# Optimization experiments

Hardware: AMD Instinct MI355X
Metric: run time of the kernel (lower is better)

The kernel has to match this reference:

```python
import jax, jax.numpy as jnp
import numpy as np

N = 8192      # nodes
IN = 1433     # input_feat_dim
H1 = 256      # hidden_dim1
H2 = 128      # hidden_dim2
EPS = 1e-5    # BatchNorm1d eps
NEG = -9e15   # GAT mask value
SLOPE = 0.2   # leaky_relu negative slope (gamma)


def setup_inputs() -> dict:
    key = jax.random.key(0)
    ks = jax.random.split(key, 8)
    x = jax.random.normal(ks[0], (N, H2), dtype=jnp.float32)
    u = jax.random.uniform(ks[1], (N, N), dtype=jnp.float32)
    adj = jnp.where(u > 0.999, jnp.float32(0.01), jnp.float32(0.0))
    def w(k, shape):
        fan = shape[0]
        return jax.random.normal(k, shape, dtype=jnp.float32) / jnp.sqrt(jnp.float32(fan))
    return {
        "x": x,
        "adj": adj,
        "W_att": w(ks[2], (H2, H2)),
        "a_att": w(ks[3], (2 * H2, 1)),
        "W_fd1": w(ks[4], (H2, H1)),
        "bn1_g": jnp.ones((H1,), jnp.float32),
        "bn1_b": jnp.zeros((H1,), jnp.float32),
        "W_fd2": w(ks[5], (H1, IN)),
        "bn2_g": jnp.ones((IN,), jnp.float32),
        "bn2_b": jnp.zeros((IN,), jnp.float32),
        "W_sd1": w(ks[6], (H2, H1)),
        "bn3_g": jnp.ones((H1,), jnp.float32),
        "bn3_b": jnp.zeros((H1,), jnp.float32),
    }


def batchnorm(h, g, b):
    # BatchNorm1d training-mode forward: batch stats, biased variance
    m = h.mean(axis=0)
    v = ((h - m) ** 2).mean(axis=0)
    return (h - m) * jax.lax.rsqrt(v + EPS) * g + b


def reference(x, adj, W_att, a_att, W_fd1, bn1_g, bn1_b, W_fd2, bn2_g, bn2_b,
              W_sd1, bn3_g, bn3_b):
    # --- GraphAttentionLayer (concat=False, dropout=0) ---
    Wh = x @ W_att                       # [N, H2]
    f1 = Wh @ a_att[:H2]                 # [N, 1]
    f2 = Wh @ a_att[H2:]                 # [N, 1]
    e = jax.nn.leaky_relu(f1 + f2.T, SLOPE)          # [N, N]
    att = jnp.where(adj > 0, e, jnp.float32(NEG))
    att = jax.nn.softmax(att, axis=1)
    z = att @ Wh                         # condensed encoder output [N, H2]
    # --- feature decoder branch ---
    h1 = jax.nn.relu(adj @ (z @ W_fd1))  # GCN: adj @ (X W), relu
    h1 = batchnorm(h1, bn1_g, bn1_b)
    feat = jax.nn.relu(adj @ (h1 @ W_fd2))
    feat = batchnorm(feat, bn2_g, bn2_b)
    # --- structure decoder branch ---
    s1 = jax.nn.relu(adj @ (z @ W_sd1))
    s1 = batchnorm(s1, bn3_g, bn3_b)
    struct = s1 @ s1.T                   # inner-product decode, identity act [N, N]
    return feat, struct
```

## Files before the change

### kernel.cpp

```cpp
#include <hip/hip_runtime.h>
#include <hip/hip_bf16.h>
#include <stdint.h>

#define NN 8192
#define MAXNZ 64
#define BN_EPS 1e-5f
#define SLOPE 0.2f
#define IND 1433
#define NPAD 1536

typedef float f32x4v __attribute__((ext_vector_type(4)));
typedef short bf16x8v __attribute__((ext_vector_type(8)));

__device__ __forceinline__ float wave_sum(float v) {
#pragma unroll
  for (int off = 32; off > 0; off >>= 1) v += __shfl_xor(v, off);
  return v;
}
__device__ __forceinline__ float wave_max(float v) {
#pragma unroll
  for (int off = 32; off > 0; off >>= 1) v = fmaxf(v, __shfl_xor(v, off));
  return v;
}

#define GLOAD_LDS16(g, l)                                                      \
  __builtin_amdgcn_global_load_lds(                                            \
      (const __attribute__((address_space(1))) unsigned int*)(g),              \
      (__attribute__((address_space(3))) unsigned int*)(l), 16, 0, 0)

__global__ __launch_bounds__(256) void prep_gemm_k(
    const float* __restrict__ A, const float* __restrict__ B,
    const float* __restrict__ aatt, const float* __restrict__ W_fd2,
    const float* __restrict__ W_fd1, const float* __restrict__ W_sd1,
    __hip_bfloat16* __restrict__ Wt, __hip_bfloat16* __restrict__ Wcatb,
    float* __restrict__ C, float* __restrict__ cs, float* __restrict__ f1,
    float* __restrict__ f2) {
  __shared__ float As[64][68];
  __shared__ float Bs[64][68];
  __shared__ float csL[64];
  const int b = blockIdx.x;
  const int t = threadIdx.x;
  if (b < NPAD) {
    int o = b * 256 + t;
    int n = o >> 8, k = o & 255;
    Wt[o] = __float2bfloat16(n < IND ? W_fd2[(size_t)k * IND + n] : 0.f);
    if (b < 256) {
      int nn = o >> 7, kk = o & 127;
      float v = nn < 256 ? W_fd1[(size_t)kk * 256 + nn]
                         : W_sd1[(size_t)kk * 256 + (nn - 256)];
      Wcatb[o] = __float2bfloat16(v);
    }
    return;
  }
  const int bx = b - NPAD;
  const int m0 = (bx & 127) * 64, n0 = (bx >> 7) * 64;
  const int tx = t & 15, ty = t >> 4;
  if (t < 64) csL[t] = 0.f;
  float acc[4][4] = {};
  for (int kt = 0; kt < 128; kt += 64) {
    if (kt) __syncthreads();
#pragma unroll
    for (int i = 0; i < 4; ++i) {
      int fid = t + 256 * i;
      int r = fid >> 4, kq = (fid & 15) * 4;
      float4 v = *(const float4*)&A[(size_t)(m0 + r) * 128 + kt + kq];
      *(float4*)&As[r][kq] = v;
    }
#pragma unroll
    for (int i = 0; i < 4; ++i) {
      int fid = t + 256 * i;
      int r = fid >> 4, cq = (fid & 15) * 4;
      float4 v = *(const float4*)&B[(size_t)(kt + r) * 128 + n0 + cq];
      *(float4*)&Bs[r][cq] = v;
    }
    __syncthreads();
#pragma unroll 4
    for (int k0 = 0; k0 < 64; k0 += 4) {
      float4 a[4], bb[4];
#pragma unroll
      for (int i = 0; i < 4; ++i) a[i] = *(const float4*)&As[ty * 4 + i][k0];
#pragma unroll
      for (int j = 0; j < 4; ++j) bb[j] = *(const float4*)&Bs[k0 + j][tx * 4];
#pragma unroll
      for (int kk = 0; kk < 4; ++kk) {
#pragma unroll
        for (int i = 0; i < 4; ++i) {
          float av = ((const float*)&a[i])[kk];
#pragma unroll
          for (int j = 0; j < 4; ++j)
            acc[i][j] += av * ((const float*)&bb[kk])[j];
        }
      }
    }
  }
#pragma unroll
  for (int i = 0; i < 4; ++i) {
    float4 v = make_float4(acc[i][0], acc[i][1], acc[i][2], acc[i][3]);
    *(float4*)&C[(size_t)(m0 + ty * 4 + i) * 128 + n0 + tx * 4] = v;
  }
  float a1v[4], a2v[4];
#pragma unroll
  for (int j = 0; j < 4; ++j) {
    a1v[j] = aatt[n0 + tx * 4 + j];
    a2v[j] = aatt[128 + n0 + tx * 4 + j];
  }
#pragma unroll
  for (int i = 0; i < 4; ++i) {
    float p1 = acc[i][0] * a1v[0] + acc[i][1] * a1v[1] + acc[i][2] * a1v[2] +
               acc[i][3] * a1v[3];
    float p2 = acc[i][0] * a2v[0] + acc[i][1] * a2v[1] + acc[i][2] * a2v[2] +
               acc[i][3] * a2v[3];
#pragma unroll
    for (int off = 1; off < 16; off <<= 1) {
      p1 += __shfl_xor(p1, off);
      p2 += __shfl_xor(p2, off);
    }
    if ((t & 15) == 0) {
      atomicAdd(&f1[m0 + ty * 4 + i], p1);
      atomicAdd(&f2[m0 + ty * 4 + i], p2);
    }
  }
  float cp[4];
#pragma unroll
  for (int j = 0; j < 4; ++j) {
    cp[j] = acc[0][j] + acc[1][j] + acc[2][j] + acc[3][j];
    cp[j] += __shfl_xor(cp[j], 16);
    cp[j] += __shfl_xor(cp[j], 32);
  }
  if ((t & 63) < 16) {
#pragma unroll
    for (int j = 0; j < 4; ++j) atomicAdd(&csL[(t & 15) * 4 + j], cp[j]);
  }
  __syncthreads();
  if (t < 64) atomicAdd(&cs[n0 + t], csL[t]);
}

__global__ void extract_attn_k(const float* __restrict__ adj, const float* __restrict__ Wh,
                               const float* __restrict__ f1, const float* __restrict__ f2,
                               const float* __restrict__ cs, int* __restrict__ nnzA,
                               int* __restrict__ idxA, float* __restrict__ valA,
                               float* __restrict__ valsumA, float* __restrict__ z) {
  __shared__ int cntL[4];
  __shared__ int idxL[4][MAXNZ];
  __shared__ float valL[4][MAXNZ];
  int l = threadIdx.x & 63, w = threadIdx.x >> 6;
  int i = blockIdx.x * 4 + w;
  if (l == 0) cntL[w] = 0;
  const float* row = adj + (size_t)i * NN;
  for (int it = 0; it < NN / 512; ++it) {
    int c0 = it * 512 + l * 8;
    float4 va = *(const float4*)&row[c0];
    float4 vb = *(const float4*)&row[c0 + 4];
    float mx = fmaxf(fmaxf(fmaxf(va.x, va.y), fmaxf(va.z, va.w)),
                     fmaxf(fmaxf(vb.x, vb.y), fmaxf(vb.z, vb.w)));
    if (mx > 0.f) {
#pragma unroll
      for (int j = 0; j < 4; ++j) {
        float v = ((const float*)&va)[j];
        if (v > 0.f) {
          int s = atomicAdd(&cntL[w], 1);
          if (s < MAXNZ) { idxL[w][s] = c0 + j; valL[w][s] = v; }
        }
      }
#pragma unroll
      for (int j = 0; j < 4; ++j) {
        float v = ((const float*)&vb)[j];
        if (v > 0.f) {
          int s = atomicAdd(&cntL[w], 1);
          if (s < MAXNZ) { idxL[w][s] = c0 + 4 + j; valL[w][s] = v; }
        }
      }
    }
  }
  int nnz = cntL[w];
  nnz = nnz < MAXNZ ? nnz : MAXNZ;
  if (l == 0) nnzA[i] = nnz;

  int c = -1;
  float v = 0.f, att = 0.f;
  if (l < nnz) { c = idxL[w][l]; v = valL[w][l]; }
  idxA[(size_t)i * MAXNZ + l] = (l < nnz) ? c : 0;
  valA[(size_t)i * MAXNZ + l] = v;
  float vs = wave_sum(v);
  if (l == 0) valsumA[i] = vs;

  if (nnz == 0) {
    const float inv = 1.0f / 8192.0f;
    z[(size_t)i * 128 + l] = cs[l] * inv;
    z[(size_t)i * 128 + 64 + l] = cs[64 + l] * inv;
    return;
  }
  float e = -INFINITY;
  if (l < nnz) {
    float u = f1[i] + f2[c];
    e = u >= 0.f ? u : SLOPE * u;
  }
  float mx = wave_max(e);
  float p = (l < nnz) ? expf(e - mx) : 0.f;
  float s = wave_sum(p);
  att = p / s;
  float a0 = 0.f, a1 = 0.f;
  for (int j = 0; j < nnz; ++j) {
    float wt = __shfl(att, j);
    int r = __shfl(c, j);
    a0 += wt * Wh[(size_t)r * 128 + l];
    a1 += wt * Wh[(size_t)r * 128 + 64 + l];
  }
  z[(size_t)i * 128 + l] = a0;
  z[(size_t)i * 128 + 64 + l] = a1;
}

__global__ void gather_z_k(const float* __restrict__ X, const int* __restrict__ nnzA,
                           const int* __restrict__ idxA, const float* __restrict__ valA,
                           __hip_bfloat16* __restrict__ Y) {
  int l = threadIdx.x & 63, w = threadIdx.x >> 6;
  int i = blockIdx.x * 4 + w;
  int nnz = nnzA[i];
  int myi = idxA[(size_t)i * MAXNZ + l];
  float myv = valA[(size_t)i * MAXNZ + l];
  float a0 = 0.f, a1 = 0.f;
  for (int j = 0; j < nnz; ++j) {
    int r = __shfl(myi, j);
    float v = __shfl(myv, j);
    a0 += v * X[(size_t)r * 128 + l];
    a1 += v * X[(size_t)r * 128 + 64 + l];
  }
  Y[(size_t)i * 128 + l] = __float2bfloat16(a0);
  Y[(size_t)i * 128 + 64 + l] = __float2bfloat16(a1);
}

__global__ void s1_gather_k(const __hip_bfloat16* __restrict__ t, const int* __restrict__ nnzA,
                            const int* __restrict__ idxA, const float* __restrict__ valA,
                            const float* __restrict__ valsumA, const float* __restrict__ sums,
                            const float* __restrict__ sumsq, const float* __restrict__ g1,
                            const float* __restrict__ b1, const float* __restrict__ g3,
                            const float* __restrict__ b3, __hip_bfloat16* __restrict__ s1b,
                            __hip_bfloat16* __restrict__ ghb) {
  __shared__ int idxL[MAXNZ];
  __shared__ float valL[MAXNZ];
  int i = blockIdx.x, tt = threadIdx.x;
  int nnz = nnzA[i];
  if (tt < MAXNZ) {
    idxL[tt] = idxA[(size_t)i * MAXNZ + tt];
    valL[tt] = valA[(size_t)i * MAXNZ + tt];
  }
  __syncthreads();
  {
    float m = sums[256 + tt] * (1.f / 8192.f);
    float va = fmaxf(sumsq[256 + tt] * (1.f / 8192.f) - m * m, 0.f);
    float sc = g3[tt] * rsqrtf(va + BN_EPS);
    float sh = b3[tt] - m * sc;
    float v = __bfloat162float(t[(size_t)i * 512 + 256 + tt]) * sc + sh;
    s1b[(size_t)i * 256 + tt] = __float2bfloat16(v);
  }
  float acc = 0.f;
  for (int j = 0; j < nnz; ++j)
    acc += valL[j] * __bfloat162float(t[(size_t)idxL[j] * 512 + tt]);
  float m = sums[tt] * (1.f / 8192.f);
  float va = fmaxf(sumsq[tt] * (1.f / 8192.f) - m * m, 0.f);
  float sc = g1[tt] * rsqrtf(va + BN_EPS);
  float sh = b1[tt] - m * sc;
  ghb[(size_t)i * 256 + tt] = __float2bfloat16(acc * sc + sh * valsumA[i]);
}

__global__ void feat_apply_k(const __hip_bfloat16* __restrict__ fp, const float* __restrict__ sums,
                             const float* __restrict__ sumsq, const float* __restrict__ g,
                             const float* __restrict__ b, float* __restrict__ out) {
  int i = blockIdx.x;
  for (int c = threadIdx.x; c < IND; c += 256) {
    float m = sums[c] * (1.f / 8192.f);
    float va = fmaxf(sumsq[c] * (1.f / 8192.f) - m * m, 0.f);
    float sc = g[c] * rsqrtf(va + BN_EPS);
    float sh = b[c] - m * sc;
    out[(size_t)i * IND + c] = __bfloat162float(fp[(size_t)i * NPAD + c]) * sc + sh;
  }
}

template <int KT>
__global__ __launch_bounds__(256) void mfma_bt_k(const short* __restrict__ A,
                                                 const short* __restrict__ Bt,
                                                 __hip_bfloat16* __restrict__ C, int ldc,
                                                 int gridN, float* __restrict__ sums,
                                                 float* __restrict__ sumsq) {
  __shared__ short lds[2][16384];
  const int nwg = gridDim.x;
  const int cpx = nwg >> 3;
  const int bid = blockIdx.x;
  const int wg = (bid & 7) * cpx + (bid >> 3);
  const int m0 = (wg / gridN) * 128, n0 = (wg % gridN) * 128;
  const int t = threadIdx.x;
  const int l = t & 63, w = t >> 6;
  const int wm = w >> 1, wn = w & 1;
  const int KW = KT * 128;
  f32x4v acc[4][4];
#pragma unroll
  for (int i = 0; i < 4; ++i)
#pragma unroll
    for (int j = 0; j < 4; ++j)
#pragma unroll
      for (int q = 0; q < 4; ++q) acc[i][j][q] = 0.f;

  for (int kt = 0; kt < KT; ++kt) {
    if (kt) __syncthreads();
#pragma unroll
    for (int i = 0; i < 8; ++i) {
      int region = w * 8 + i;
      int lr = region * 4 + (l >> 4);
      int ch = (l & 15) ^ (lr & 7);
      const short* gA = A + ((size_t)(m0 + lr) * KW + kt * 128 + ch * 8);
      GLOAD_LDS16(gA, &lds[0][region * 512]);
      const short* gB = Bt + ((size_t)(n0 + lr) * KW + kt * 128 + ch * 8);
      GLOAD_LDS16(gB, &lds[1][region * 512]);
    }
    __syncthreads();
#pragma unroll
    for (int ks = 0; ks < 4; ++ks) {
      bf16x8v af[4], bf[4];
#pragma unroll
      for (int mi = 0; mi < 4; ++mi) {
        int lr = wm * 64 + mi * 16 + (l & 15);
        int ch = (ks * 4 + (l >> 4)) ^ (lr & 7);
        af[mi] = *(const bf16x8v*)&lds[0][lr * 128 + ch * 8];
      }
#pragma unroll
      for (int nj = 0; nj < 4; ++nj) {
        int lr = wn * 64 + nj * 16 + (l & 15);
        int ch = (ks * 4 + (l >> 4)) ^ (lr & 7);
        bf[nj] = *(const bf16x8v*)&lds[1][lr * 128 + ch * 8];
      }
#pragma unroll
      for (int mi = 0; mi < 4; ++mi)
#pragma unroll
        for (int nj = 0; nj < 4; ++nj)
          acc[mi][nj] = __builtin_amdgcn_mfma_f32_16x16x32_bf16(
              af[mi], bf[nj], acc[mi][nj], 0, 0, 0);
    }
  }
#pragma unroll
  for (int nj = 0; nj < 4; ++nj) {
    int col = n0 + wn * 64 + nj * 16 + (l & 15);
    float s = 0.f, ss = 0.f;
#pragma unroll
    for (int mi = 0; mi < 4; ++mi) {
#pragma unroll
      for (int q = 0; q < 4; ++q) {
        int row = m0 + wm * 64 + mi * 16 + (l >> 4) * 4 + q;
        float v = fmaxf(acc[mi][nj][q], 0.f);
        C[(size_t)row * ldc + col] = __float2bfloat16(v);
        s += v;
        ss += v * v;
      }
    }
    s += __shfl_xor(s, 16);
    s += __shfl_xor(s, 32);
    ss += __shfl_xor(ss, 16);
    ss += __shfl_xor(ss, 32);
    if ((l >> 4) == 0) {
      atomicAdd(&sums[col], s);
      atomicAdd(&sumsq[col], ss);
    }
  }
}

__global__ __launch_bounds__(256) void tail_k(const short* __restrict__ Agh,
                                              const short* __restrict__ Wt,
                                              __hip_bfloat16* __restrict__ featb,
                                              float* __restrict__ sums,
                                              float* __restrict__ sumsq,
                                              const short* __restrict__ S,
                                              float* __restrict__ C) {
  __shared__ short lds[2][16384];
  const int bid = blockIdx.x;
  const int fA = bid * 24 / 89;
  const int fB = (bid + 1) * 24 / 89;
  const bool isFeat = fB > fA;
  const int t = threadIdx.x;
  const int l = t & 63, w = t >> 6;
  const int wm = w >> 1, wn = w & 1;
  f32x4v acc[4][4];
#pragma unroll
  for (int i = 0; i < 4; ++i)
#pragma unroll
    for (int j = 0; j < 4; ++j)
#pragma unroll
      for (int q = 0; q < 4; ++q) acc[i][j][q] = 0.f;

  if (isFeat) {
    const int fb = fA;
    const int wg = (fb & 7) * 96 + (fb >> 3);
    const int m0 = (wg / 12) * 128, n0 = (wg % 12) * 128;
    for (int kt = 0; kt < 2; ++kt) {
      if (kt) __syncthreads();
#pragma unroll
      for (int i = 0; i < 8; ++i) {
        int region = w * 8 + i;
        int lr = region * 4 + (l >> 4);
        int ch = (l & 15) ^ (lr & 7);
        const short* gA = Agh + ((size_t)(m0 + lr) * 256 + kt * 128 + ch * 8);
        GLOAD_LDS16(gA, &lds[0][region * 512]);
        const short* gB = Wt + ((size_t)(n0 + lr) * 256 + kt * 128 + ch * 8);
        GLOAD_LDS16(gB, &lds[1][region * 512]);
      }
      __syncthreads();
#pragma unroll
      for (int ks = 0; ks < 4; ++ks) {
        bf16x8v af[4], bf[4];
#pragma unroll
        for (int mi = 0; mi < 4; ++mi) {
          int lr = wm * 64 + mi * 16 + (l & 15);
          int ch = (ks * 4 + (l >> 4)) ^ (lr & 7);
          af[mi] = *(const bf16x8v*)&lds[0][lr * 128 + ch * 8];
        }
#pragma unroll
        for (int nj = 0; nj < 4; ++nj) {
          int lr = wn * 64 + nj * 16 + (l & 15);
          int ch = (ks * 4 + (l >> 4)) ^ (lr & 7);
          bf[nj] = *(const bf16x8v*)&lds[1][lr * 128 + ch * 8];
        }
#pragma unroll
        for (int mi = 0; mi < 4; ++mi)
#pragma unroll
          for (int nj = 0; nj < 4; ++nj)
            acc[mi][nj] = __builtin_amdgcn_mfma_f32_16x16x32_bf16(
                af[mi], bf[nj], acc[mi][nj], 0, 0, 0);
      }
    }
#pragma unroll
    for (int nj = 0; nj < 4; ++nj) {
      int col = n0 + wn * 64 + nj * 16 + (l & 15);
      float s = 0.f, ss = 0.f;
#pragma unroll
      for (int mi = 0; mi < 4; ++mi) {
#pragma unroll
        for (int q = 0; q < 4; ++q) {
          int row = m0 + wm * 64 + mi * 16 + (l >> 4) * 4 + q;
          float v = fmaxf(acc[mi][nj][q], 0.f);
          featb[(size_t)row * NPAD + col] = __float2bfloat16(v);
          s += v;
          ss += v * v;
        }
      }
      s += __shfl_xor(s, 16);
      s += __shfl_xor(s, 32);
      ss += __shfl_xor(ss, 16);
      ss += __shfl_xor(ss, 32);
      if ((l >> 4) == 0) {
        atomicAdd(&sums[col], s);
        atomicAdd(&sumsq[col], ss);
      }
    }
  } else {
    const int sb = bid - fA;
    const int wg = (sb & 7) * 260 + (sb >> 3);
    int bi = (int)((129.0f - sqrtf(16641.0f - 8.0f * (float)wg)) * 0.5f);
    while ((bi + 1) * 64 - ((bi + 1) * bi) / 2 <= wg) ++bi;
    while (bi * 64 - (bi * (bi - 1)) / 2 > wg) --bi;
    const int bj = bi + (wg - (bi * 64 - (bi * (bi - 1)) / 2));
    const int m0 = bi * 128, n0 = bj * 128;
    for (int kt = 0; kt < 2; ++kt) {
      if (kt) __syncthreads();
#pragma unroll
      for (int i = 0; i < 8; ++i) {
        int region = w * 8 + i;
        int lr = region * 4 + (l >> 4);
        int ch = (l & 15) ^ (lr & 7);
        const short* gA = S + ((size_t)(m0 + lr) * 256 + kt * 128 + ch * 8);
        GLOAD_LDS16(gA, &lds[0][region * 512]);
        const short* gB = S + ((size_t)(n0 + lr) * 256 + kt * 128 + ch * 8);
        GLOAD_LDS16(gB, &lds[1][region * 512]);
      }
      __syncthreads();
#pragma unroll
      for (int ks = 0; ks < 4; ++ks) {
        bf16x8v af[4], bf[4];
#pragma unroll
        for (int mi = 0; mi < 4; ++mi) {
          int lr = wm * 64 + mi * 16 + (l & 15);
          int ch = (ks * 4 + (l >> 4)) ^ (lr & 7);
          af[mi] = *(const bf16x8v*)&lds[0][lr * 128 + ch * 8];
        }
#pragma unroll
        for (int nj = 0; nj < 4; ++nj) {
          int lr = wn * 64 + nj * 16 + (l & 15);
          int ch = (ks * 4 + (l >> 4)) ^ (lr & 7);
          bf[nj] = *(const bf16x8v*)&lds[1][lr * 128 + ch * 8];
        }
#pragma unroll
        for (int mi = 0; mi < 4; ++mi)
#pragma unroll
          for (int nj = 0; nj < 4; ++nj)
            acc[mi][nj] = __builtin_amdgcn_mfma_f32_16x16x32_bf16(
                af[mi], bf[nj], acc[mi][nj], 0, 0, 0);
      }
    }
#pragma unroll
    for (int mi = 0; mi < 4; ++mi) {
#pragma unroll
      for (int nj = 0; nj < 4; ++nj) {
        int col = n0 + wn * 64 + nj * 16 + (l & 15);
#pragma unroll
        for (int q = 0; q < 4; ++q) {
          int row = m0 + wm * 64 + mi * 16 + (l >> 4) * 4 + q;
          C[(size_t)row * NN + col] = acc[mi][nj][q];
        }
      }
    }
    if (bi != bj) {
#pragma unroll
      for (int nj = 0; nj < 4; ++nj) {
        int col = n0 + wn * 64 + nj * 16 + (l & 15);
#pragma unroll
        for (int mi = 0; mi < 4; ++mi) {
          int row0 = m0 + wm * 64 + mi * 16 + (l >> 4) * 4;
          float4 v = make_float4(acc[mi][nj][0], acc[mi][nj][1], acc[mi][nj][2],
                                 acc[mi][nj][3]);
          *(float4*)&C[(size_t)col * NN + row0] = v;
        }
      }
    }
  }
}

extern "C" void kernel_launch(void* const* d_in, const int* in_sizes, int n_in,
                              void* d_out, int out_size, void* d_ws, size_t ws_size,
                              hipStream_t stream) {
  const float* x = (const float*)d_in[0];
  const float* adj = (const float*)d_in[1];
  const float* W_att = (const float*)d_in[2];
  const float* a_att = (const float*)d_in[3];
  const float* W_fd1 = (const float*)d_in[4];
  const float* bn1g = (const float*)d_in[5];
  const float* bn1b = (const float*)d_in[6];
  const float* W_fd2 = (const float*)d_in[7];
  const float* bn2g = (const float*)d_in[8];
  const float* bn2b = (const float*)d_in[9];
  const float* W_sd1 = (const float*)d_in[10];
  const float* bn3g = (const float*)d_in[11];
  const float* bn3b = (const float*)d_in[12];

  float* out = (float*)d_out;
  float* feat_out = out;
  float* struct_out = out + (size_t)NN * IND;

  float* ws = (float*)d_ws;
  size_t off = 0;
  auto alloc = [&](size_t nfloats) {
    float* p = ws + off;
    off += (nfloats + 255) & ~(size_t)255;
    return p;
  };
  float* Wh = alloc((size_t)NN * 128);
  float* z = alloc((size_t)NN * 128);
  float* valsum = alloc(NN);
  const size_t ZTOT = 256 + 8192 + 8192 + 512 + 512 + 1536 + 1536;
  float* zbase = alloc(ZTOT);
  float* cs = zbase;
  float* f1 = zbase + 256;
  float* f2 = zbase + 256 + 8192;
  float* sumsA = zbase + 256 + 16384;
  float* sumsqA = sumsA + 512;
  float* sumsB = sumsqA + 512;
  float* sumsqB = sumsB + 1536;
  float* valA = alloc((size_t)NN * MAXNZ);
  int* idxA = (int*)alloc((size_t)NN * MAXNZ);
  int* nnzA = (int*)alloc(NN);
  __hip_bfloat16* tbuf = (__hip_bfloat16*)alloc((size_t)NN * 256);
  __hip_bfloat16* gb = (__hip_bfloat16*)alloc((size_t)NN * 64);
  __hip_bfloat16* s1b = (__hip_bfloat16*)alloc((size_t)NN * 128);
  __hip_bfloat16* ghb = (__hip_bfloat16*)alloc((size_t)NN * 128);
  __hip_bfloat16* Wt = (__hip_bfloat16*)alloc((size_t)NPAD * 128);
  __hip_bfloat16* Wcatb = (__hip_bfloat16*)alloc(512 * 64);
  __hip_bfloat16* featb = (__hip_bfloat16*)alloc((size_t)NN * NPAD / 2);

  hipMemsetAsync(zbase, 0, ZTOT * sizeof(float), stream);

  prep_gemm_k<<<NPAD + 256, 256, 0, stream>>>(x, W_att, a_att, W_fd2, W_fd1, W_sd1,
                                              Wt, Wcatb, Wh, cs, f1, f2);

  extract_attn_k<<<NN / 4, 256, 0, stream>>>(adj, Wh, f1, f2, cs, nnzA, idxA, valA,
                                             valsum, z);
  gather_z_k<<<NN / 4, 256, 0, stream>>>(z, nnzA, idxA, valA, gb);

  mfma_bt_k<1><<<64 * 4, 256, 0, stream>>>((const short*)gb, (const short*)Wcatb,
                                           tbuf, 512, 4, sumsA, sumsqA);
  s1_gather_k<<<NN, 256, 0, stream>>>(tbuf, nnzA, idxA, valA, valsum, sumsA, sumsqA,
                                      bn1g, bn1b, bn3g, bn3b, s1b, ghb);

  tail_k<<<2848, 256, 0, stream>>>((const short*)ghb, (const short*)Wt, featb,
                                   sumsB, sumsqB, (const short*)s1b, struct_out);
  feat_apply_k<<<NN, 256, 0, stream>>>(featb, sumsB, sumsqB, bn2g, bn2b, feat_out);
}
```

Before: 249.7 us.

## Fuse adjacency scan into head kernel alongside Wh GEMM; store z as packed bf16

The adjacency row scan that builds the sparse row lists moves into the same launch as the x@W_att GEMM and the weight transposes, so the 256 MB adj read can overlap the small GEMM instead of waiting for it. Attention softmax and z aggregation become a separate kernel that reads the extracted lists. z is stored as packed bf16 pairs, halving its traffic in the following gather. Splitting the attention step out adds a launch and reloads idx/nnz from global, and bf16 z slightly reduces precision before the next gather.

```diff
diff --git a/kernel.cpp b/kernel.cpp
--- a/kernel.cpp
+++ b/kernel.cpp
@@ -11,6 +11,7 @@
 
 typedef float f32x4v __attribute__((ext_vector_type(4)));
 typedef short bf16x8v __attribute__((ext_vector_type(8)));
+typedef unsigned int uint;
 
 __device__ __forceinline__ float wave_sum(float v) {
 #pragma unroll
@@ -21,6 +22,22 @@
 #pragma unroll
   for (int off = 32; off > 0; off >>= 1) v = fmaxf(v, __shfl_xor(v, off));
   return v;
+}
+__device__ __forceinline__ float bflo(uint u) {
+  union { uint x; float f; } c;
+  c.x = u << 16;
+  return c.f;
+}
+__device__ __forceinline__ float bfhi(uint u) {
+  union { uint x; float f; } c;
+  c.x = u & 0xffff0000u;
+  return c.f;
+}
+__device__ __forceinline__ uint packbf(float a, float b) {
+  union { __hip_bfloat16 h; unsigned short u; } ca, cb;
+  ca.h = __float2bfloat16(a);
+  cb.h = __float2bfloat16(b);
+  return (uint)ca.u | ((uint)cb.u << 16);
 }
 
 #define GLOAD_LDS16(g, l)                                                      \
@@ -28,23 +45,98 @@
       (const __attribute__((address_space(1))) unsigned int*)(g),              \
       (__attribute__((address_space(3))) unsigned int*)(l), 16, 0, 0)
 
-__global__ __launch_bounds__(256) void prep_gemm_k(
-    const float* __restrict__ A, const float* __restrict__ B,
-    const float* __restrict__ aatt, const float* __restrict__ W_fd2,
-    const float* __restrict__ W_fd1, const float* __restrict__ W_sd1,
-    __hip_bfloat16* __restrict__ Wt, __hip_bfloat16* __restrict__ Wcatb,
-    float* __restrict__ C, float* __restrict__ cs, float* __restrict__ f1,
-    float* __restrict__ f2) {
-  __shared__ float As[64][68];
-  __shared__ float Bs[64][68];
-  __shared__ float csL[64];
+__global__ __launch_bounds__(256) void head_k(
+    const float* __restrict__ adj, const float* __restrict__ x,
+    const float* __restrict__ W_att, const float* __restrict__ aatt,
+    const float* __restrict__ W_fd2, const float* __restrict__ W_fd1,
+    const float* __restrict__ W_sd1, __hip_bfloat16* __restrict__ Wt,
+    __hip_bfloat16* __restrict__ Wcatb, float* __restrict__ Wh,
+    float* __restrict__ cs, float* __restrict__ f1, float* __restrict__ f2,
+    int* __restrict__ nnzA, int* __restrict__ idxA, float* __restrict__ valA,
+    float* __restrict__ valsumA) {
+  __shared__ union {
+    struct {
+      float As[64][68];
+      float Bs[64][68];
+      float csL[64];
+    } g0;
+    struct {
+      int cnt[4];
+      int idx[4][MAXNZ];
+      float val[4][MAXNZ];
+    } ex;
+  } sh;
   const int b = blockIdx.x;
   const int t = threadIdx.x;
-  if (b < NPAD) {
-    int o = b * 256 + t;
+  const int l = t & 63, w = t >> 6;
+
+  if (b < 2048) {
+    const int i = b * 4 + w;
+    if (l == 0) sh.ex.cnt[w] = 0;
+    const float* row = adj + (size_t)i * NN;
+    auto push4 = [&](const float4& vv, int base) {
+#pragma unroll
+      for (int j = 0; j < 4; ++j) {
+        float pv = ((const float*)&vv)[j];
+        if (pv > 0.f) {
+          int s = atomicAdd(&sh.ex.cnt[w], 1);
+          if (s < MAXNZ) {
+            sh.ex.idx[w][s] = base + j;
+            sh.ex.val[w][s] = pv;
+          }
+        }
+      }
+    };
+    for (int it = 0; it < 4; ++it) {
+      int c0 = it * 2048 + l * 32;
+      float4 v0 = *(const float4*)&row[c0];
+      float4 v1 = *(const float4*)&row[c0 + 4];
+      float4 v2 = *(const float4*)&row[c0 + 8];
+      float4 v3 = *(const float4*)&row[c0 + 12];
+      float4 v4 = *(const float4*)&row[c0 + 16];
+      float4 v5 = *(const float4*)&row[c0 + 20];
+      float4 v6 = *(const float4*)&row[c0 + 24];
+      float4 v7 = *(const float4*)&row[c0 + 28];
+      float m0 = fmaxf(fmaxf(fmaxf(v0.x, v0.y), fmaxf(v0.z, v0.w)),
+                       fmaxf(fmaxf(v1.x, v1.y), fmaxf(v1.z, v1.w)));
+      float m1 = fmaxf(fmaxf(fmaxf(v2.x, v2.y), fmaxf(v2.z, v2.w)),
+                       fmaxf(fmaxf(v3.x, v3.y), fmaxf(v3.z, v3.w)));
+      float m2 = fmaxf(fmaxf(fmaxf(v4.x, v4.y), fmaxf(v4.z, v4.w)),
+                       fmaxf(fmaxf(v5.x, v5.y), fmaxf(v5.z, v5.w)));
+      float m3 = fmaxf(fmaxf(fmaxf(v6.x, v6.y), fmaxf(v6.z, v6.w)),
+                       fmaxf(fmaxf(v7.x, v7.y), fmaxf(v7.z, v7.w)));
+      if (fmaxf(fmaxf(m0, m1), fmaxf(m2, m3)) > 0.f) {
+        push4(v0, c0);
+        push4(v1, c0 + 4);
+        push4(v2, c0 + 8);
+        push4(v3, c0 + 12);
+        push4(v4, c0 + 16);
+        push4(v5, c0 + 20);
+        push4(v6, c0 + 24);
+        push4(v7, c0 + 28);
+      }
+    }
+    int nnz = sh.ex.cnt[w];
+    nnz = nnz < MAXNZ ? nnz : MAXNZ;
+    if (l == 0) nnzA[i] = nnz;
+    int c = 0;
+    float v = 0.f;
+    if (l < nnz) {
+      c = sh.ex.idx[w][l];
+      v = sh.ex.val[w][l];
+    }
+    idxA[(size_t)i * MAXNZ + l] = c;
+    valA[(size_t)i * MAXNZ + l] = v;
+    float vs = wave_sum(v);
+    if (l == 0) valsumA[i] = vs;
+    return;
+  }
+  if (b < 2048 + NPAD) {
+    int job = b - 2048;
+    int o = job * 256 + t;
     int n = o >> 8, k = o & 255;
     Wt[o] = __float2bfloat16(n < IND ? W_fd2[(size_t)k * IND + n] : 0.f);
-    if (b < 256) {
+    if (job < 256) {
       int nn = o >> 7, kk = o & 127;
       float v = nn < 256 ? W_fd1[(size_t)kk * 256 + nn]
                          : W_sd1[(size_t)kk * 256 + (nn - 256)];
@@ -52,10 +144,10 @@
     }
     return;
   }
-  const int bx = b - NPAD;
+  const int bx = b - 2048 - NPAD;
   const int m0 = (bx & 127) * 64, n0 = (bx >> 7) * 64;
   const int tx = t & 15, ty = t >> 4;
-  if (t < 64) csL[t] = 0.f;
+  if (t < 64) sh.g0.csL[t] = 0.f;
   float acc[4][4] = {};
   for (int kt = 0; kt < 128; kt += 64) {
     if (kt) __syncthreads();
@@ -63,24 +155,24 @@
     for (int i = 0; i < 4; ++i) {
       int fid = t + 256 * i;
       int r = fid >> 4, kq = (fid & 15) * 4;
-      float4 v = *(const float4*)&A[(size_t)(m0 + r) * 128 + kt + kq];
-      *(float4*)&As[r][kq] = v;
+      float4 v = *(const float4*)&x[(size_t)(m0 + r) * 128 + kt + kq];
+      *(float4*)&sh.g0.As[r][kq] = v;
     }
 #pragma unroll
     for (int i = 0; i < 4; ++i) {
       int fid = t + 256 * i;
       int r = fid >> 4, cq = (fid & 15) * 4;
-      float4 v = *(const float4*)&B[(size_t)(kt + r) * 128 + n0 + cq];
-      *(float4*)&Bs[r][cq] = v;
+      float4 v = *(const float4*)&W_att[(size_t)(kt + r) * 128 + n0 + cq];
+      *(float4*)&sh.g0.Bs[r][cq] = v;
     }
     __syncthreads();
 #pragma unroll 4
     for (int k0 = 0; k0 < 64; k0 += 4) {
       float4 a[4], bb[4];
 #pragma unroll
-      for (int i = 0; i < 4; ++i) a[i] = *(const float4*)&As[ty * 4 + i][k0];
-#pragma unroll
-      for (int j = 0; j < 4; ++j) bb[j] = *(const float4*)&Bs[k0 + j][tx * 4];
+      for (int i = 0; i < 4; ++i) a[i] = *(const float4*)&sh.g0.As[ty * 4 + i][k0];
+#pragma unroll
+      for (int j = 0; j < 4; ++j) bb[j] = *(const float4*)&sh.g0.Bs[k0 + j][tx * 4];
 #pragma unroll
       for (int kk = 0; kk < 4; ++kk) {
 #pragma unroll
@@ -96,7 +188,7 @@
 #pragma unroll
   for (int i = 0; i < 4; ++i) {
     float4 v = make_float4(acc[i][0], acc[i][1], acc[i][2], acc[i][3]);
-    *(float4*)&C[(size_t)(m0 + ty * 4 + i) * 128 + n0 + tx * 4] = v;
+    *(float4*)&Wh[(size_t)(m0 + ty * 4 + i) * 128 + n0 + tx * 4] = v;
   }
   float a1v[4], a2v[4];
 #pragma unroll
@@ -129,67 +221,25 @@
   }
   if ((t & 63) < 16) {
 #pragma unroll
-    for (int j = 0; j < 4; ++j) atomicAdd(&csL[(t & 15) * 4 + j], cp[j]);
+    for (int j = 0; j < 4; ++j) atomicAdd(&sh.g0.csL[(t & 15) * 4 + j], cp[j]);
   }
   __syncthreads();
-  if (t < 64) atomicAdd(&cs[n0 + t], csL[t]);
-}
-
-__global__ void extract_attn_k(const float* __restrict__ adj, const float* __restrict__ Wh,
-                               const float* __restrict__ f1, const float* __restrict__ f2,
-                               const float* __restrict__ cs, int* __restrict__ nnzA,
-                               int* __restrict__ idxA, float* __restrict__ valA,
-                               float* __restrict__ valsumA, float* __restrict__ z) {
-  __shared__ int cntL[4];
-  __shared__ int idxL[4][MAXNZ];
-  __shared__ float valL[4][MAXNZ];
+  if (t < 64) atomicAdd(&cs[n0 + t], sh.g0.csL[t]);
+}
+
+__global__ void attn_z_k(const float* __restrict__ Wh, const float* __restrict__ f1,
+                         const float* __restrict__ f2, const float* __restrict__ cs,
+                         const int* __restrict__ nnzA, const int* __restrict__ idxA,
+                         const float* __restrict__ valA, uint* __restrict__ zp) {
   int l = threadIdx.x & 63, w = threadIdx.x >> 6;
   int i = blockIdx.x * 4 + w;
-  if (l == 0) cntL[w] = 0;
-  const float* row = adj + (size_t)i * NN;
-  for (int it = 0; it < NN / 512; ++it) {
-    int c0 = it * 512 + l * 8;
-    float4 va = *(const float4*)&row[c0];
-    float4 vb = *(const float4*)&row[c0 + 4];
-    float mx = fmaxf(fmaxf(fmaxf(va.x, va.y), fmaxf(va.z, va.w)),
-                     fmaxf(fmaxf(vb.x, vb.y), fmaxf(vb.z, vb.w)));
-    if (mx > 0.f) {
-#pragma unroll
-      for (int j = 0; j < 4; ++j) {
-        float v = ((const float*)&va)[j];
-        if (v > 0.f) {
-          int s = atomicAdd(&cntL[w], 1);
-          if (s < MAXNZ) { idxL[w][s] = c0 + j; valL[w][s] = v; }
-        }
-      }
-#pragma unroll
-      for (int j = 0; j < 4; ++j) {
-        float v = ((const float*)&vb)[j];
-        if (v > 0.f) {
-          int s = atomicAdd(&cntL[w], 1);
-          if (s < MAXNZ) { idxL[w][s] = c0 + 4 + j; valL[w][s] = v; }
-        }
-      }
-    }
-  }
-  int nnz = cntL[w];
-  nnz = nnz < MAXNZ ? nnz : MAXNZ;
-  if (l == 0) nnzA[i] = nnz;
-
-  int c = -1;
-  float v = 0.f, att = 0.f;
-  if (l < nnz) { c = idxL[w][l]; v = valL[w][l]; }
-  idxA[(size_t)i * MAXNZ + l] = (l < nnz) ? c : 0;
-  valA[(size_t)i * MAXNZ + l] = v;
-  float vs = wave_sum(v);
-  if (l == 0) valsumA[i] = vs;
-
+  int nnz = nnzA[i];
   if (nnz == 0) {
     const float inv = 1.0f / 8192.0f;
-    z[(size_t)i * 128 + l] = cs[l] * inv;
-    z[(size_t)i * 128 + 64 + l] = cs[64 + l] * inv;
+    zp[(size_t)i * 64 + l] = packbf(cs[2 * l] * inv, cs[2 * l + 1] * inv);
     return;
   }
+  int c = (l < nnz) ? idxA[(size_t)i * MAXNZ + l] : 0;
   float e = -INFINITY;
   if (l < nnz) {
     float u = f1[i] + f2[c];
@@ -198,21 +248,21 @@
   float mx = wave_max(e);
   float p = (l < nnz) ? expf(e - mx) : 0.f;
   float s = wave_sum(p);
-  att = p / s;
+  float att = p / s;
   float a0 = 0.f, a1 = 0.f;
   for (int j = 0; j < nnz; ++j) {
     float wt = __shfl(att, j);
     int r = __shfl(c, j);
-    a0 += wt * Wh[(size_t)r * 128 + l];
-    a1 += wt * Wh[(size_t)r * 128 + 64 + l];
-  }
-  z[(size_t)i * 128 + l] = a0;
-  z[(size_t)i * 128 + 64 + l] = a1;
-}
-
-__global__ void gather_z_k(const float* __restrict__ X, const int* __restrict__ nnzA,
+    float2 wv = *(const float2*)&Wh[(size_t)r * 128 + 2 * l];
+    a0 += wt * wv.x;
+    a1 += wt * wv.y;
+  }
+  zp[(size_t)i * 64 + l] = packbf(a0, a1);
+}
+
+__global__ void gather_z_k(const uint* __restrict__ zp, const int* __restrict__ nnzA,
                            const int* __restrict__ idxA, const float* __restrict__ valA,
-                           __hip_bfloat16* __restrict__ Y) {
+                           uint* __restrict__ gbp) {
   int l = threadIdx.x & 63, w = threadIdx.x >> 6;
   int i = blockIdx.x * 4 + w;
   int nnz = nnzA[i];
@@ -222,58 +272,11 @@
   for (int j = 0; j < nnz; ++j) {
     int r = __shfl(myi, j);
     float v = __shfl(myv, j);
-    a0 += v * X[(size_t)r * 128 + l];
-    a1 += v * X[(size_t)r * 128 + 64 + l];
-  }
-  Y[(size_t)i * 128 + l] = __float2bfloat16(a0);
-  Y[(size_t)i * 128 + 64 + l] = __float2bfloat16(a1);
-}
-
-__global__ void s1_gather_k(const __hip_bfloat16* __restrict__ t, const int* __restrict__ nnzA,
-                            const int* __restrict__ idxA, const float* __restrict__ valA,
-                            const float* __restrict__ valsumA, const float* __restrict__ sums,
-                            const float* __restrict__ sumsq, const float* __restrict__ g1,
-                            const float* __restrict__ b1, const float* __restrict__ g3,
-                            const float* __restrict__ b3, __hip_bfloat16* __restrict__ s1b,
-                            __hip_bfloat16* __restrict__ ghb) {
-  __shared__ int idxL[MAXNZ];
-  __shared__ float valL[MAXNZ];
-  int i = blockIdx.x, tt = threadIdx.x;
-  int nnz = nnzA[i];
-  if (tt < MAXNZ) {
-    idxL[tt] = idxA[(size_t)i * MAXNZ + tt];
-    valL[tt] = valA[(size_t)i * MAXNZ + tt];
-  }
-  __syncthreads();
-  {
-    float m = sums[256 + tt] * (1.f / 8192.f);
-    float va = fmaxf(sumsq[256 + tt] * (1.f / 8192.f) - m * m, 0.f);
-    float sc = g3[tt] * rsqrtf(va + BN_EPS);
-    float sh = b3[tt] - m * sc;
-    float v = __bfloat162float(t[(size_t)i * 512 + 256 + tt]) * sc + sh;
-    s1b[(size_t)i * 256 + tt] = __float2bfloat16(v);
-  }
-  float acc = 0.f;
-  for (int j = 0; j < nnz; ++j)
-    acc += valL[j] * __bfloat162float(t[(size_t)idxL[j] * 512 + tt]);
-  float m = sums[tt] * (1.f / 8192.f);
-  float va = fmaxf(sumsq[tt] * (1.f / 8192.f) - m * m, 0.f);
-  float sc = g1[tt] * rsqrtf(va + BN_EPS);
-  float sh = b1[tt] - m * sc;
-  ghb[(size_t)i * 256 + tt] = __float2bfloat16(acc * sc + sh * valsumA[i]);
-}
-
-__global__ void feat_apply_k(const __hip_bfloat16* __restrict__ fp, const float* __restrict__ sums,
-                             const float* __restrict__ sumsq, const float* __restrict__ g,
-                             const float* __restrict__ b, float* __restrict__ out) {
-  int i = blockIdx.x;
-  for (int c = threadIdx.x; c < IND; c += 256) {
-    float m = sums[c] * (1.f / 8192.f);
-    float va = fmaxf(sumsq[c] * (1.f / 8192.f) - m * m, 0.f);
-    float sc = g[c] * rsqrtf(va + BN_EPS);
-    float sh = b[c] - m * sc;
-    out[(size_t)i * IND + c] = __bfloat162float(fp[(size_t)i * NPAD + c]) * sc + sh;
-  }
+    uint pv = zp[(size_t)r * 64 + l];
+    a0 += v * bflo(pv);
+    a1 += v * bfhi(pv);
+  }
+  gbp[(size_t)i * 64 + l] = packbf(a0, a1);
 }
 
 template <int KT>
@@ -362,6 +365,40 @@
   }
 }
 
+__global__ void s1_gather_k(const __hip_bfloat16* __restrict__ t, const int* __restrict__ nnzA,
+                            const int* __restrict__ idxA, const float* __restrict__ valA,
+                            const float* __restrict__ valsumA, const float* __restrict__ sums,
+                            const float* __restrict__ sumsq, const float* __restrict__ g1,
+                            const float* __restrict__ b1, const float* __restrict__ g3,
+                            const float* __restrict__ b3, __hip_bfloat16* __restrict__ s1b,
+                            __hip_bfloat16* __restrict__ ghb) {
+  __shared__ int idxL[MAXNZ];
+  __shared__ float valL[MAXNZ];
+  int i = blockIdx.x, tt = threadIdx.x;
+  int nnz = nnzA[i];
+  if (tt < MAXNZ) {
+    idxL[tt] = idxA[(size_t)i * MAXNZ + tt];
+    valL[tt] = valA[(size_t)i * MAXNZ + tt];
+  }
+  __syncthreads();
+  {
+    float m = sums[256 + tt] * (1.f / 8192.f);
+    float va = fmaxf(sumsq[256 + tt] * (1.f / 8192.f) - m * m, 0.f);
+    float sc = g3[tt] * rsqrtf(va + BN_EPS);
+    float sh = b3[tt] - m * sc;
+    float v = __bfloat162float(t[(size_t)i * 512 + 256 + tt]) * sc + sh;
+    s1b[(size_t)i * 256 + tt] = __float2bfloat16(v);
+  }
+  float acc = 0.f;
+  for (int j = 0; j < nnz; ++j)
+    acc += valL[j] * __bfloat162float(t[(size_t)idxL[j] * 512 + tt]);
+  float m = sums[tt] * (1.f / 8192.f);
+  float va = fmaxf(sumsq[tt] * (1.f / 8192.f) - m * m, 0.f);
+  float sc = g1[tt] * rsqrtf(va + BN_EPS);
+  float sh = b1[tt] - m * sc;
+  ghb[(size_t)i * 256 + tt] = __float2bfloat16(acc * sc + sh * valsumA[i]);
+}
+
 __global__ __launch_bounds__(256) void tail_k(const short* __restrict__ Agh,
                                               const short* __restrict__ Wt,
                                               __hip_bfloat16* __restrict__ featb,
@@ -521,6 +558,19 @@
   }
 }
 
+__global__ void feat_apply_k(const __hip_bfloat16* __restrict__ fp, const float* __restrict__ sums,
+                             const float* __restrict__ sumsq, const float* __restrict__ g,
+                             const float* __restrict__ b, float* __restrict__ out) {
+  int i = blockIdx.x;
+  for (int c = threadIdx.x; c < IND; c += 256) {
+    float m = sums[c] * (1.f / 8192.f);
+    float va = fmaxf(sumsq[c] * (1.f / 8192.f) - m * m, 0.f);
+    float sc = g[c] * rsqrtf(va + BN_EPS);
+    float sh = b[c] - m * sc;
+    out[(size_t)i * IND + c] = __bfloat162float(fp[(size_t)i * NPAD + c]) * sc + sh;
+  }
+}
+
 extern "C" void kernel_launch(void* const* d_in, const int* in_sizes, int n_in,
                               void* d_out, int out_size, void* d_ws, size_t ws_size,
                               hipStream_t stream) {
@@ -550,14 +600,14 @@
     return p;
   };
   float* Wh = alloc((size_t)NN * 128);
-  float* z = alloc((size_t)NN * 128);
+  uint* zp = (uint*)alloc((size_t)NN * 64);
   float* valsum = alloc(NN);
   const size_t ZTOT = 256 + 8192 + 8192 + 512 + 512 + 1536 + 1536;
   float* zbase = alloc(ZTOT);
   float* cs = zbase;
   float* f1 = zbase + 256;
-  float* f2 = zbase + 256 + 8192;
-  float* sumsA = zbase + 256 + 16384;
+  float* f2 = f1 + 8192;
+  float* sumsA = f2 + 8192;
   float* sumsqA = sumsA + 512;
   float* sumsB = sumsqA + 512;
   float* sumsqB = sumsB + 1536;
@@ -565,7 +615,7 @@
   int* idxA = (int*)alloc((size_t)NN * MAXNZ);
   int* nnzA = (int*)alloc(NN);
   __hip_bfloat16* tbuf = (__hip_bfloat16*)alloc((size_t)NN * 256);
-  __hip_bfloat16* gb = (__hip_bfloat16*)alloc((size_t)NN * 64);
+  uint* gbp = (uint*)alloc((size_t)NN * 64);
   __hip_bfloat16* s1b = (__hip_bfloat16*)alloc((size_t)NN * 128);
   __hip_bfloat16* ghb = (__hip_bfloat16*)alloc((size_t)NN * 128);
   __hip_bfloat16* Wt = (__hip_bfloat16*)alloc((size_t)NPAD * 128);
@@ -574,18 +624,15 @@
 
   hipMemsetAsync(zbase, 0, ZTOT * sizeof(float), stream);
 
-  prep_gemm_k<<<NPAD + 256, 256, 0, stream>>>(x, W_att, a_att, W_fd2, W_fd1, W_sd1,
-                                              Wt, Wcatb, Wh, cs, f1, f2);
-
-  extract_attn_k<<<NN / 4, 256, 0, stream>>>(adj, Wh, f1, f2, cs, nnzA, idxA, valA,
-                                             valsum, z);
-  gather_z_k<<<NN / 4, 256, 0, stream>>>(z, nnzA, idxA, valA, gb);
-
-  mfma_bt_k<1><<<64 * 4, 256, 0, stream>>>((const short*)gb, (const short*)Wcatb,
+  head_k<<<2048 + NPAD + 256, 256, 0, stream>>>(adj, x, W_att, a_att, W_fd2,
+                                                W_fd1, W_sd1, Wt, Wcatb, Wh, cs,
+                                                f1, f2, nnzA, idxA, valA, valsum);
+  attn_z_k<<<NN / 4, 256, 0, stream>>>(Wh, f1, f2, cs, nnzA, idxA, valA, zp);
+  gather_z_k<<<NN / 4, 256, 0, stream>>>(zp, nnzA, idxA, valA, gbp);
+  mfma_bt_k<1><<<64 * 4, 256, 0, stream>>>((const short*)gbp, (const short*)Wcatb,
                                            tbuf, 512, 4, sumsA, sumsqA);
   s1_gather_k<<<NN, 256, 0, stream>>>(tbuf, nnzA, idxA, valA, valsum, sumsA, sumsqA,
                                       bn1g, bn1b, bn3g, bn3b, s1b, ghb);
-
   tail_k<<<2848, 256, 0, stream>>>((const short*)ghb, (const short*)Wt, featb,
                                    sumsB, sumsqB, (const short*)s1b, struct_out);
   feat_apply_k<<<NN, 256, 0, stream>>>(featb, sumsB, sumsqB, bn2g, bn2b, feat_out);
```

Result: slower. 261.1 us (+4.6%).
